# Kernel tuning notes

Measured on AMD Instinct MI355X. Metric: run time of the kernel, lower is better.

The kernel has to match this reference:

```python
import jax, jax.numpy as jnp
import numpy as np
import math

ROPE_BASE = 10000.0
ALIBI_SLOPE = 2.0 ** (-8.0)  # _get_alibi_slopes(1) == [2**(-8*1/1)]


def _rope_cos_sin(T, d):
    inv_freq = 1.0 / (ROPE_BASE ** (jnp.arange(0, d, 2, dtype=jnp.float32) / d))
    t = jnp.arange(T, dtype=jnp.float32)
    freqs = jnp.einsum('i,j->ij', t, inv_freq)          # [T, d/2]
    emb = jnp.concatenate([freqs, freqs], axis=-1)      # [T, d]
    return jnp.cos(emb), jnp.sin(emb)


def _rotate_half(x):
    x1, x2 = jnp.split(x, 2, axis=-1)
    return jnp.concatenate([-x2, x1], axis=-1)


def setup_inputs() -> dict:
    key = jax.random.key(0)
    kq, kk, kv = jax.random.split(key, 3)
    B, T, H = 8, 2048, 256
    return {
        'q': jax.random.normal(kq, (B, T, H), dtype=jnp.float32),
        'k': jax.random.normal(kk, (B, T, H), dtype=jnp.float32),
        'v': jax.random.normal(kv, (B, T, H), dtype=jnp.float32),
    }


def reference(q, k, v):
    B, T, H = q.shape  # num_heads == 1, so head_dim == H
    cos, sin = _rope_cos_sin(T, H)                      # [T, H]
    qe = q * cos + _rotate_half(q) * sin                # [B, T, H]
    ke = k * cos + _rotate_half(k) * sin                # [B, T, H]

    scale = 1.0 / math.sqrt(H)
    scores = jnp.einsum('btd,bsd->bts', qe, ke) * scale  # [B, T, T]

    pos = jnp.arange(T)
    rel = (pos[None, :] - pos[:, None]).astype(jnp.float32)  # [T, T]
    alibi = (ALIBI_SLOPE * rel)[None, None, :, :]            # [1, 1, T, T]

    # torch broadcast: [B,T,T] + [1,1,T,T] -> [1,B,T,T]
    scores = scores + alibi
    attn = jax.nn.softmax(scores, axis=-1)              # [1, B, T, T]
    out = jnp.matmul(attn, v)                           # [1, B, T, H]
    return out
```

## Files before the change

kernel.cpp:

```cpp
#include <hip/hip_runtime.h>

#define B_ 8
#define T_ 2048
#define H_ 256
#define PSTR 40
#define SCALE2 0.0901684403f
#define SLOPE2 0.00563552752f

typedef __attribute__((ext_vector_type(8))) short bf16x8;
typedef __attribute__((ext_vector_type(4))) float f32x4;

#define MFMA16(a, b, c) __builtin_amdgcn_mfma_f32_16x16x32_bf16((a), (b), (c), 0, 0, 0)

__device__ __forceinline__ ushort f2bf(float f) {
  unsigned u = __float_as_uint(f);
  u += 0x7FFFu + ((u >> 16) & 1u);
  return (ushort)(u >> 16);
}

__device__ __forceinline__ void gl_lds16(const ushort* g, ushort* l) {
  __builtin_amdgcn_global_load_lds(
      (const __attribute__((address_space(1))) unsigned int*)g,
      (__attribute__((address_space(3))) unsigned int*)l, 16, 0, 0);
}

__global__ void prep_kernel(const float* __restrict__ k, const float* __restrict__ v,
                            ushort* __restrict__ kt, ushort* __restrict__ vt) {
  __shared__ ushort tile[64][72];
  const int bid = blockIdx.x;
  const int tid = threadIdx.x;
  if (bid < 4096) {
    int idx = bid * 256 + tid;
    int jp = idx & 63, bt = idx >> 6;
    int t = bt & (T_ - 1);
    int b = bt >> 11;
    int j = jp * 2;
    float rv0 = (float)t * exp2f((float)j * -0.103810252959f) * 0.15915494309f;
    float rv1 = (float)t * exp2f((float)(j + 1) * -0.103810252959f) * 0.15915494309f;
    float fr0 = rv0 - floorf(rv0), fr1 = rv1 - floorf(rv1);
    float sn0 = __builtin_amdgcn_sinf(fr0), cs0 = __builtin_amdgcn_cosf(fr0);
    float sn1 = __builtin_amdgcn_sinf(fr1), cs1 = __builtin_amdgcn_cosf(fr1);
    size_t base = (size_t)bt * H_ + j;
    float2 a = *(const float2*)(k + base);
    float2 c = *(const float2*)(k + base + 128);
    ushort2 lo, hi;
    lo.x = f2bf(a.x * cs0 - c.x * sn0); lo.y = f2bf(a.y * cs1 - c.y * sn1);
    hi.x = f2bf(c.x * cs0 + a.x * sn0); hi.y = f2bf(c.y * cs1 + a.y * sn1);
    size_t kdst = (((size_t)(b * 64 + (t >> 5)) * 32 + (j >> 3)) * 32 + (t & 31)) * 8 + (j & 7);
    *(ushort2*)(kt + kdst) = lo;
    *(ushort2*)(kt + kdst + 4096) = hi;
  } else {
    int bid2 = bid - 4096;
    int b = bid2 >> 7, rem = bid2 & 127;
    int h0 = (rem >> 5) * 64, t0 = (rem & 31) * 64;
    int c4 = tid & 15, r0 = tid >> 4;
#pragma unroll
    for (int p = 0; p < 4; ++p) {
      int row = r0 + p * 16;
      const float4 f = *(const float4*)(v + ((size_t)(b * T_ + t0 + row)) * H_ + h0 + c4 * 4);
      ushort4 u;
      u.x = f2bf(f.x); u.y = f2bf(f.y); u.z = f2bf(f.z); u.w = f2bf(f.w);
      *(ushort4*)&tile[row][(c4 * 4) ^ (8 * ((row >> 3) & 7))] = u;
    }
    __syncthreads();
#pragma unroll
    for (int p = 0; p < 2; ++p) {
      int c = tid + p * 256;
      int h = c >> 3, tc = (c & 7) * 8;
      int xo = 8 * (c & 7);
      ushort4 u0, u1;
      u0.x = tile[tc + 0][h ^ xo]; u0.y = tile[tc + 1][h ^ xo];
      u0.z = tile[tc + 2][h ^ xo]; u0.w = tile[tc + 3][h ^ xo];
      u1.x = tile[tc + 4][h ^ xo]; u1.y = tile[tc + 5][h ^ xo];
      u1.z = tile[tc + 6][h ^ xo]; u1.w = tile[tc + 7][h ^ xo];
      int tg = t0 + tc;
      size_t dst = (((size_t)(b * 64 + (tg >> 5)) * 4 + ((tg >> 3) & 3)) * 256 + (h0 + h)) * 8;
      *(ushort4*)(vt + dst) = u0;
      *(ushort4*)(vt + dst + 4) = u1;
    }
  }
}

__global__ __launch_bounds__(128, 1)
void attn_kernel(const float* __restrict__ q, const ushort* __restrict__ kt,
                 const ushort* __restrict__ vt, float* __restrict__ out,
                 float* __restrict__ o1, float* __restrict__ lpart) {
  __shared__ ushort Ksh[2][8192];
  __shared__ ushort Vsh[8192];
  __shared__ ushort Psh[2][32 * PSTR];

  const int tid = threadIdx.x;
  const int w = tid >> 6, lane = tid & 63, quad = lane >> 4, l16 = lane & 15;
  const int b = blockIdx.x;
  const int q0 = blockIdx.y * 64;
  const int sp = blockIdx.z;
  const int kvb = sp * (T_ / 2);

  bf16x8 aq[2][8];
  {
    const float* qb = q + ((size_t)(b * T_) + q0 + w * 32) * H_;
#pragma unroll
    for (int mt = 0; mt < 2; ++mt) {
      int t = q0 + w * 32 + mt * 16 + l16;
      float qv[8][8];
#pragma unroll
      for (int ks = 0; ks < 8; ++ks) {
        float4 x0 = *(const float4*)(qb + (size_t)(mt * 16 + l16) * H_ + ks * 32 + quad * 8);
        float4 x1 = *(const float4*)(qb + (size_t)(mt * 16 + l16) * H_ + ks * 32 + quad * 8 + 4);
        qv[ks][0] = x0.x; qv[ks][1] = x0.y; qv[ks][2] = x0.z; qv[ks][3] = x0.w;
        qv[ks][4] = x1.x; qv[ks][5] = x1.y; qv[ks][6] = x1.z; qv[ks][7] = x1.w;
      }
#pragma unroll
      for (int ks = 0; ks < 4; ++ks)
#pragma unroll
        for (int e = 0; e < 8; ++e) {
          int d = ks * 32 + quad * 8 + e;
          float rv = (float)t * exp2f((float)d * -0.103810252959f) * 0.15915494309f;
          float fr = rv - floorf(rv);
          float sn = __builtin_amdgcn_sinf(fr), cs = __builtin_amdgcn_cosf(fr);
          aq[mt][ks][e]     = (short)f2bf(qv[ks][e] * cs - qv[ks + 4][e] * sn);
          aq[mt][ks + 4][e] = (short)f2bf(qv[ks + 4][e] * cs + qv[ks][e] * sn);
        }
    }
  }

  const f32x4 fzero = {0.f, 0.f, 0.f, 0.f};
  f32x4 O[2][16], lac[2];
#pragma unroll
  for (int mt = 0; mt < 2; ++mt) {
    lac[mt] = fzero;
#pragma unroll
    for (int ht = 0; ht < 16; ++ht) O[mt][ht] = fzero;
  }
  bf16x8 vones;
#pragma unroll
  for (int i = 0; i < 8; ++i) vones[i] = (short)0x3F80;

  const ushort* ktb = kt + (size_t)(b * 64 + sp * 32) * 8192;
  const ushort* vtb = vt + (size_t)(b * 64 + sp * 32) * 8192;
  const int stoff = w * 4096 + lane * 8;

#pragma unroll
  for (int i = 0; i < 8; ++i)
    gl_lds16(ktb + stoff + i * 512, &Ksh[0][stoff + i * 512]);
  __builtin_amdgcn_sched_barrier(0);
  __builtin_amdgcn_s_waitcnt(0x0070);
  __builtin_amdgcn_s_barrier();
  __builtin_amdgcn_sched_barrier(0);

  const float arb = SLOPE2 * (float)(q0 + w * 32 + quad * 4);

  for (int it = 0; it < 32; ++it) {
    const int p = it & 1;
    {
      const ushort* vg = vtb + (size_t)it * 8192;
#pragma unroll
      for (int i = 0; i < 8; ++i)
        gl_lds16(vg + stoff + i * 512, &Vsh[stoff + i * 512]);
      const int itn = (it < 31) ? it + 1 : 31;
      const ushort* kg = ktb + (size_t)itn * 8192;
#pragma unroll
      for (int i = 0; i < 8; ++i)
        gl_lds16(kg + stoff + i * 512, &Ksh[1 - p][stoff + i * 512]);
    }
    __builtin_amdgcn_sched_barrier(0);

    f32x4 s[2][2] = {{fzero, fzero}, {fzero, fzero}};
#pragma unroll
    for (int ks = 0; ks < 8; ++ks)
#pragma unroll
      for (int nt = 0; nt < 2; ++nt) {
        bf16x8 kf = *(const bf16x8*)&Ksh[p][((ks * 4 + quad) * 32 + nt * 16 + l16) * 8];
        s[0][nt] = MFMA16(aq[0][ks], kf, s[0][nt]);
        s[1][nt] = MFMA16(aq[1][ks], kf, s[1][nt]);
      }

    __builtin_amdgcn_sched_barrier(0);
    __builtin_amdgcn_s_waitcnt(0x0F78);
    __builtin_amdgcn_s_barrier();
    __builtin_amdgcn_sched_barrier(0);

#pragma unroll
    for (int nt = 0; nt < 2; ++nt) {
      float ac = SLOPE2 * (float)(kvb + it * 32 + nt * 16 + l16);
#pragma unroll
      for (int mt = 0; mt < 2; ++mt)
#pragma unroll
        for (int r = 0; r < 4; ++r) {
          float a0 = ac - arb - SLOPE2 * (float)(mt * 16 + r);
          float pv = __builtin_amdgcn_exp2f(fmaf(s[mt][nt][r], SCALE2, a0));
          Psh[w][(mt * 16 + quad * 4 + r) * PSTR + nt * 16 + l16] = f2bf(pv);
        }
    }

    bf16x8 pf0 = *(const bf16x8*)&Psh[w][l16 * PSTR + quad * 8];
    bf16x8 pf1 = *(const bf16x8*)&Psh[w][(16 + l16) * PSTR + quad * 8];
    lac[0] = MFMA16(pf0, vones, lac[0]);
    lac[1] = MFMA16(pf1, vones, lac[1]);
#pragma unroll
    for (int ht = 0; ht < 16; ++ht) {
      bf16x8 vf = *(const bf16x8*)&Vsh[(quad * 256 + ht * 16 + l16) * 8];
      O[0][ht] = MFMA16(pf0, vf, O[0][ht]);
      O[1][ht] = MFMA16(pf1, vf, O[1][ht]);
    }

    __builtin_amdgcn_sched_barrier(0);
    __builtin_amdgcn_s_waitcnt(0x0070);
    __builtin_amdgcn_s_barrier();
    __builtin_amdgcn_sched_barrier(0);
  }

  float* od = (sp == 0) ? out : o1;
  float* ob = od + ((size_t)(b * T_) + q0 + w * 32) * H_;
#pragma unroll
  for (int mt = 0; mt < 2; ++mt)
#pragma unroll
    for (int r = 0; r < 4; ++r) {
      int row = mt * 16 + quad * 4 + r;
#pragma unroll
      for (int ht = 0; ht < 16; ++ht)
        ob[(size_t)row * H_ + ht * 16 + l16] = O[mt][ht][r];
    }
  if (l16 == 0) {
#pragma unroll
    for (int mt = 0; mt < 2; ++mt)
#pragma unroll
      for (int r = 0; r < 4; ++r)
        lpart[(size_t)(sp * B_ + b) * T_ + q0 + w * 32 + mt * 16 + quad * 4 + r] =
            lac[mt][r];
  }
}

__global__ void combine_kernel(float* __restrict__ out, const float* __restrict__ o1,
                               const float* __restrict__ lpart) {
  int idx = blockIdx.x * 256 + threadIdx.x;
  int row = idx >> 6;
  float inv = 1.0f / (lpart[row] + lpart[B_ * T_ + row]);
  float4 a = ((const float4*)out)[idx];
  float4 c = ((const float4*)o1)[idx];
  a.x = (a.x + c.x) * inv; a.y = (a.y + c.y) * inv;
  a.z = (a.z + c.z) * inv; a.w = (a.w + c.w) * inv;
  ((float4*)out)[idx] = a;
}

extern "C" void kernel_launch(void* const* d_in, const int* in_sizes, int n_in,
                              void* d_out, int out_size, void* d_ws, size_t ws_size,
                              hipStream_t stream) {
  const float* q = (const float*)d_in[0];
  const float* k = (const float*)d_in[1];
  const float* v = (const float*)d_in[2];
  float* out = (float*)d_out;

  const size_t elems = (size_t)B_ * T_ * H_;
  ushort* kt = (ushort*)d_ws;
  ushort* vt = kt + elems;
  float* o1 = (float*)(vt + elems);
  float* lpart = o1 + elems;

  prep_kernel<<<dim3(5120), 256, 0, stream>>>(k, v, kt, vt);
  attn_kernel<<<dim3(B_, T_ / 64, 2), 128, 0, stream>>>(q, kt, vt, out, o1, lpart);
  combine_kernel<<<dim3((B_ * T_ * H_ / 4) / 256), 256, 0, stream>>>(out, o1, lpart);
}
```

Before: 164.8 us.

## Use 8-wave blocks of 128 queries with double-buffered K/V prefetch

The attention kernel moves from 2 waves covering 64 query rows, 32 rows each, to 8 waves covering 128 query rows, 16 rows each. Each K/V tile loaded into LDS is now shared by four times as many query rows. V is now double-buffered like K, and tiles are prefetched two iterations ahead, leaving one barrier per iteration instead of two. The price is more LDS, fewer MFMAs per LDS fragment read since each wave handles one 16-row tile, and half as many blocks in the grid (256).

```diff
diff --git a/kernel.cpp b/kernel.cpp
--- a/kernel.cpp
+++ b/kernel.cpp
@@ -81,153 +81,134 @@
   }
 }
 
-__global__ __launch_bounds__(128, 1)
+__global__ __launch_bounds__(512, 2)
 void attn_kernel(const float* __restrict__ q, const ushort* __restrict__ kt,
                  const ushort* __restrict__ vt, float* __restrict__ out,
                  float* __restrict__ o1, float* __restrict__ lpart) {
   __shared__ ushort Ksh[2][8192];
-  __shared__ ushort Vsh[8192];
-  __shared__ ushort Psh[2][32 * PSTR];
+  __shared__ ushort Vsh[2][8192];
+  __shared__ ushort Psh[8][16 * PSTR];
 
   const int tid = threadIdx.x;
   const int w = tid >> 6, lane = tid & 63, quad = lane >> 4, l16 = lane & 15;
   const int b = blockIdx.x;
-  const int q0 = blockIdx.y * 64;
+  const int q0 = blockIdx.y * 128;
   const int sp = blockIdx.z;
   const int kvb = sp * (T_ / 2);
 
-  bf16x8 aq[2][8];
+  bf16x8 aq[8];
   {
-    const float* qb = q + ((size_t)(b * T_) + q0 + w * 32) * H_;
-#pragma unroll
-    for (int mt = 0; mt < 2; ++mt) {
-      int t = q0 + w * 32 + mt * 16 + l16;
-      float qv[8][8];
-#pragma unroll
-      for (int ks = 0; ks < 8; ++ks) {
-        float4 x0 = *(const float4*)(qb + (size_t)(mt * 16 + l16) * H_ + ks * 32 + quad * 8);
-        float4 x1 = *(const float4*)(qb + (size_t)(mt * 16 + l16) * H_ + ks * 32 + quad * 8 + 4);
-        qv[ks][0] = x0.x; qv[ks][1] = x0.y; qv[ks][2] = x0.z; qv[ks][3] = x0.w;
-        qv[ks][4] = x1.x; qv[ks][5] = x1.y; qv[ks][6] = x1.z; qv[ks][7] = x1.w;
+    const float* qb = q + ((size_t)(b * T_) + q0 + w * 16) * H_;
+    const int t = q0 + w * 16 + l16;
+    float qv[8][8];
+#pragma unroll
+    for (int ks = 0; ks < 8; ++ks) {
+      float4 x0 = *(const float4*)(qb + (size_t)l16 * H_ + ks * 32 + quad * 8);
+      float4 x1 = *(const float4*)(qb + (size_t)l16 * H_ + ks * 32 + quad * 8 + 4);
+      qv[ks][0] = x0.x; qv[ks][1] = x0.y; qv[ks][2] = x0.z; qv[ks][3] = x0.w;
+      qv[ks][4] = x1.x; qv[ks][5] = x1.y; qv[ks][6] = x1.z; qv[ks][7] = x1.w;
+    }
+#pragma unroll
+    for (int ks = 0; ks < 4; ++ks)
+#pragma unroll
+      for (int e = 0; e < 8; ++e) {
+        int d = ks * 32 + quad * 8 + e;
+        float rv = (float)t * exp2f((float)d * -0.103810252959f) * 0.15915494309f;
+        float fr = rv - floorf(rv);
+        float sn = __builtin_amdgcn_sinf(fr), cs = __builtin_amdgcn_cosf(fr);
+        aq[ks][e]     = (short)f2bf(qv[ks][e] * cs - qv[ks + 4][e] * sn);
+        aq[ks + 4][e] = (short)f2bf(qv[ks + 4][e] * cs + qv[ks][e] * sn);
       }
-#pragma unroll
-      for (int ks = 0; ks < 4; ++ks)
-#pragma unroll
-        for (int e = 0; e < 8; ++e) {
-          int d = ks * 32 + quad * 8 + e;
-          float rv = (float)t * exp2f((float)d * -0.103810252959f) * 0.15915494309f;
-          float fr = rv - floorf(rv);
-          float sn = __builtin_amdgcn_sinf(fr), cs = __builtin_amdgcn_cosf(fr);
-          aq[mt][ks][e]     = (short)f2bf(qv[ks][e] * cs - qv[ks + 4][e] * sn);
-          aq[mt][ks + 4][e] = (short)f2bf(qv[ks + 4][e] * cs + qv[ks][e] * sn);
-        }
-    }
   }
 
   const f32x4 fzero = {0.f, 0.f, 0.f, 0.f};
-  f32x4 O[2][16], lac[2];
-#pragma unroll
-  for (int mt = 0; mt < 2; ++mt) {
-    lac[mt] = fzero;
-#pragma unroll
-    for (int ht = 0; ht < 16; ++ht) O[mt][ht] = fzero;
-  }
+  f32x4 O[16], lac = fzero;
+#pragma unroll
+  for (int ht = 0; ht < 16; ++ht) O[ht] = fzero;
   bf16x8 vones;
 #pragma unroll
   for (int i = 0; i < 8; ++i) vones[i] = (short)0x3F80;
 
   const ushort* ktb = kt + (size_t)(b * 64 + sp * 32) * 8192;
   const ushort* vtb = vt + (size_t)(b * 64 + sp * 32) * 8192;
-  const int stoff = w * 4096 + lane * 8;
-
-#pragma unroll
-  for (int i = 0; i < 8; ++i)
-    gl_lds16(ktb + stoff + i * 512, &Ksh[0][stoff + i * 512]);
-  __builtin_amdgcn_sched_barrier(0);
-  __builtin_amdgcn_s_waitcnt(0x0070);
-  __builtin_amdgcn_s_barrier();
-  __builtin_amdgcn_sched_barrier(0);
-
-  const float arb = SLOPE2 * (float)(q0 + w * 32 + quad * 4);
+  const int stoff = tid * 8;
+
+#pragma unroll
+  for (int tt = 0; tt < 2; ++tt) {
+    const ushort* kg = ktb + (size_t)tt * 8192;
+    const ushort* vg = vtb + (size_t)tt * 8192;
+    gl_lds16(kg + stoff, &Ksh[tt][stoff]);
+    gl_lds16(kg + stoff + 4096, &Ksh[tt][stoff + 4096]);
+    gl_lds16(vg + stoff, &Vsh[tt][stoff]);
+    gl_lds16(vg + stoff + 4096, &Vsh[tt][stoff + 4096]);
+  }
+
+  const float arb = SLOPE2 * (float)(q0 + w * 16 + quad * 4);
 
   for (int it = 0; it < 32; ++it) {
     const int p = it & 1;
-    {
-      const ushort* vg = vtb + (size_t)it * 8192;
-#pragma unroll
-      for (int i = 0; i < 8; ++i)
-        gl_lds16(vg + stoff + i * 512, &Vsh[stoff + i * 512]);
-      const int itn = (it < 31) ? it + 1 : 31;
-      const ushort* kg = ktb + (size_t)itn * 8192;
-#pragma unroll
-      for (int i = 0; i < 8; ++i)
-        gl_lds16(kg + stoff + i * 512, &Ksh[1 - p][stoff + i * 512]);
-    }
-    __builtin_amdgcn_sched_barrier(0);
-
-    f32x4 s[2][2] = {{fzero, fzero}, {fzero, fzero}};
+    __builtin_amdgcn_sched_barrier(0);
+    if (it == 31) __builtin_amdgcn_s_waitcnt(0x0070);
+    else          __builtin_amdgcn_s_waitcnt(0x0F74);
+    __builtin_amdgcn_s_barrier();
+    __builtin_amdgcn_sched_barrier(0);
+
+    f32x4 s[2] = {fzero, fzero};
 #pragma unroll
     for (int ks = 0; ks < 8; ++ks)
 #pragma unroll
       for (int nt = 0; nt < 2; ++nt) {
         bf16x8 kf = *(const bf16x8*)&Ksh[p][((ks * 4 + quad) * 32 + nt * 16 + l16) * 8];
-        s[0][nt] = MFMA16(aq[0][ks], kf, s[0][nt]);
-        s[1][nt] = MFMA16(aq[1][ks], kf, s[1][nt]);
+        s[nt] = MFMA16(aq[ks], kf, s[nt]);
       }
-
-    __builtin_amdgcn_sched_barrier(0);
-    __builtin_amdgcn_s_waitcnt(0x0F78);
-    __builtin_amdgcn_s_barrier();
-    __builtin_amdgcn_sched_barrier(0);
 
 #pragma unroll
     for (int nt = 0; nt < 2; ++nt) {
       float ac = SLOPE2 * (float)(kvb + it * 32 + nt * 16 + l16);
 #pragma unroll
-      for (int mt = 0; mt < 2; ++mt)
-#pragma unroll
-        for (int r = 0; r < 4; ++r) {
-          float a0 = ac - arb - SLOPE2 * (float)(mt * 16 + r);
-          float pv = __builtin_amdgcn_exp2f(fmaf(s[mt][nt][r], SCALE2, a0));
-          Psh[w][(mt * 16 + quad * 4 + r) * PSTR + nt * 16 + l16] = f2bf(pv);
-        }
-    }
-
-    bf16x8 pf0 = *(const bf16x8*)&Psh[w][l16 * PSTR + quad * 8];
-    bf16x8 pf1 = *(const bf16x8*)&Psh[w][(16 + l16) * PSTR + quad * 8];
-    lac[0] = MFMA16(pf0, vones, lac[0]);
-    lac[1] = MFMA16(pf1, vones, lac[1]);
+      for (int r = 0; r < 4; ++r) {
+        float a0 = ac - arb - SLOPE2 * (float)r;
+        float pv = __builtin_amdgcn_exp2f(fmaf(s[nt][r], SCALE2, a0));
+        Psh[w][(quad * 4 + r) * PSTR + nt * 16 + l16] = f2bf(pv);
+      }
+    }
+
+    bf16x8 pf = *(const bf16x8*)&Psh[w][l16 * PSTR + quad * 8];
+    lac = MFMA16(pf, vones, lac);
 #pragma unroll
     for (int ht = 0; ht < 16; ++ht) {
-      bf16x8 vf = *(const bf16x8*)&Vsh[(quad * 256 + ht * 16 + l16) * 8];
-      O[0][ht] = MFMA16(pf0, vf, O[0][ht]);
-      O[1][ht] = MFMA16(pf1, vf, O[1][ht]);
-    }
-
-    __builtin_amdgcn_sched_barrier(0);
-    __builtin_amdgcn_s_waitcnt(0x0070);
+      bf16x8 vf = *(const bf16x8*)&Vsh[p][(quad * 256 + ht * 16 + l16) * 8];
+      O[ht] = MFMA16(pf, vf, O[ht]);
+    }
+
+    __builtin_amdgcn_sched_barrier(0);
+    __builtin_amdgcn_s_waitcnt(0xC07F);
     __builtin_amdgcn_s_barrier();
     __builtin_amdgcn_sched_barrier(0);
+
+    if (it < 30) {
+      const ushort* kg = ktb + (size_t)(it + 2) * 8192;
+      const ushort* vg = vtb + (size_t)(it + 2) * 8192;
+      gl_lds16(kg + stoff, &Ksh[p][stoff]);
+      gl_lds16(kg + stoff + 4096, &Ksh[p][stoff + 4096]);
+      gl_lds16(vg + stoff, &Vsh[p][stoff]);
+      gl_lds16(vg + stoff + 4096, &Vsh[p][stoff + 4096]);
+    }
   }
 
   float* od = (sp == 0) ? out : o1;
-  float* ob = od + ((size_t)(b * T_) + q0 + w * 32) * H_;
-#pragma unroll
-  for (int mt = 0; mt < 2; ++mt)
-#pragma unroll
-    for (int r = 0; r < 4; ++r) {
-      int row = mt * 16 + quad * 4 + r;
-#pragma unroll
-      for (int ht = 0; ht < 16; ++ht)
-        ob[(size_t)row * H_ + ht * 16 + l16] = O[mt][ht][r];
-    }
+  float* ob = od + ((size_t)(b * T_) + q0 + w * 16) * H_;
+#pragma unroll
+  for (int r = 0; r < 4; ++r) {
+    int row = quad * 4 + r;
+#pragma unroll
+    for (int ht = 0; ht < 16; ++ht)
+      ob[(size_t)row * H_ + ht * 16 + l16] = O[ht][r];
+  }
   if (l16 == 0) {
 #pragma unroll
-    for (int mt = 0; mt < 2; ++mt)
-#pragma unroll
-      for (int r = 0; r < 4; ++r)
-        lpart[(size_t)(sp * B_ + b) * T_ + q0 + w * 32 + mt * 16 + quad * 4 + r] =
-            lac[mt][r];
+    for (int r = 0; r < 4; ++r)
+      lpart[(size_t)(sp * B_ + b) * T_ + q0 + w * 16 + quad * 4 + r] = lac[r];
   }
 }
 
@@ -258,6 +239,6 @@
   float* lpart = o1 + elems;
 
   prep_kernel<<<dim3(5120), 256, 0, stream>>>(k, v, kt, vt);
-  attn_kernel<<<dim3(B_, T_ / 64, 2), 128, 0, stream>>>(q, kt, vt, out, o1, lpart);
+  attn_kernel<<<dim3(B_, T_ / 128, 2), 512, 0, stream>>>(q, kt, vt, out, o1, lpart);
   combine_kernel<<<dim3((B_ * T_ * H_ / 4) / 256), 256, 0, stream>>>(out, o1, lpart);
 }
```

After: 151.5 us. 8.1% less time.

## Double-buffer K/V with 4-wave blocks, split-KV into 4, vectorize K prep

Applied to the files above, without the earlier changes.

Attention blocks grow to four waves covering 128 query rows. K and V are both double-buffered and prefetched two tiles ahead, with a single barrier per iteration and s_setprio raised around the MFMA bursts. The KV dimension is split into up to four parts when workspace allows, and the combine kernel sums a variable number of partials. K rotary prep now handles eight elements per thread with 16-byte stores. The aim is better latency hiding and occupancy, at the cost of more LDS per block and extra partial-output traffic in combine.

```diff
diff --git a/kernel.cpp b/kernel.cpp
--- a/kernel.cpp
+++ b/kernel.cpp
@@ -6,6 +6,7 @@
 #define PSTR 40
 #define SCALE2 0.0901684403f
 #define SLOPE2 0.00563552752f
+#define ELEMS ((size_t)B_ * T_ * H_)
 
 typedef __attribute__((ext_vector_type(8))) short bf16x8;
 typedef __attribute__((ext_vector_type(4))) float f32x4;
@@ -29,28 +30,34 @@
   __shared__ ushort tile[64][72];
   const int bid = blockIdx.x;
   const int tid = threadIdx.x;
-  if (bid < 4096) {
+  if (bid < 1024) {
     int idx = bid * 256 + tid;
-    int jp = idx & 63, bt = idx >> 6;
+    int d8 = idx & 15;
+    int bt = idx >> 4;
     int t = bt & (T_ - 1);
     int b = bt >> 11;
-    int j = jp * 2;
-    float rv0 = (float)t * exp2f((float)j * -0.103810252959f) * 0.15915494309f;
-    float rv1 = (float)t * exp2f((float)(j + 1) * -0.103810252959f) * 0.15915494309f;
-    float fr0 = rv0 - floorf(rv0), fr1 = rv1 - floorf(rv1);
-    float sn0 = __builtin_amdgcn_sinf(fr0), cs0 = __builtin_amdgcn_cosf(fr0);
-    float sn1 = __builtin_amdgcn_sinf(fr1), cs1 = __builtin_amdgcn_cosf(fr1);
-    size_t base = (size_t)bt * H_ + j;
-    float2 a = *(const float2*)(k + base);
-    float2 c = *(const float2*)(k + base + 128);
-    ushort2 lo, hi;
-    lo.x = f2bf(a.x * cs0 - c.x * sn0); lo.y = f2bf(a.y * cs1 - c.y * sn1);
-    hi.x = f2bf(c.x * cs0 + a.x * sn0); hi.y = f2bf(c.y * cs1 + a.y * sn1);
-    size_t kdst = (((size_t)(b * 64 + (t >> 5)) * 32 + (j >> 3)) * 32 + (t & 31)) * 8 + (j & 7);
-    *(ushort2*)(kt + kdst) = lo;
-    *(ushort2*)(kt + kdst + 4096) = hi;
+    size_t base = (size_t)bt * H_ + d8 * 8;
+    float4 a0 = *(const float4*)(k + base);
+    float4 a1 = *(const float4*)(k + base + 4);
+    float4 c0 = *(const float4*)(k + base + 128);
+    float4 c1 = *(const float4*)(k + base + 132);
+    float av[8] = {a0.x, a0.y, a0.z, a0.w, a1.x, a1.y, a1.z, a1.w};
+    float cv[8] = {c0.x, c0.y, c0.z, c0.w, c1.x, c1.y, c1.z, c1.w};
+    bf16x8 lo, hi;
+#pragma unroll
+    for (int e = 0; e < 8; ++e) {
+      int j = d8 * 8 + e;
+      float rv = (float)t * exp2f((float)j * -0.103810252959f) * 0.15915494309f;
+      float fr = rv - floorf(rv);
+      float sn = __builtin_amdgcn_sinf(fr), cs = __builtin_amdgcn_cosf(fr);
+      lo[e] = (short)f2bf(av[e] * cs - cv[e] * sn);
+      hi[e] = (short)f2bf(cv[e] * cs + av[e] * sn);
+    }
+    size_t kdst = (((size_t)(b * 64 + (t >> 5)) * 32 + d8) * 32 + (t & 31)) * 8;
+    *(bf16x8*)(kt + kdst) = lo;
+    *(bf16x8*)(kt + kdst + 4096) = hi;
   } else {
-    int bid2 = bid - 4096;
+    int bid2 = bid - 1024;
     int b = bid2 >> 7, rem = bid2 & 127;
     int h0 = (rem >> 5) * 64, t0 = (rem & 31) * 64;
     int c4 = tid & 15, r0 = tid >> 4;
@@ -81,20 +88,22 @@
   }
 }
 
-__global__ __launch_bounds__(128, 1)
+__global__ __launch_bounds__(256, 2)
 void attn_kernel(const float* __restrict__ q, const ushort* __restrict__ kt,
                  const ushort* __restrict__ vt, float* __restrict__ out,
-                 float* __restrict__ o1, float* __restrict__ lpart) {
+                 float* __restrict__ opart, float* __restrict__ lpart) {
   __shared__ ushort Ksh[2][8192];
-  __shared__ ushort Vsh[8192];
-  __shared__ ushort Psh[2][32 * PSTR];
+  __shared__ ushort Vsh[2][8192];
+  __shared__ ushort Psh[4][32 * PSTR];
 
   const int tid = threadIdx.x;
   const int w = tid >> 6, lane = tid & 63, quad = lane >> 4, l16 = lane & 15;
   const int b = blockIdx.x;
-  const int q0 = blockIdx.y * 64;
+  const int q0 = blockIdx.y * 128;
   const int sp = blockIdx.z;
-  const int kvb = sp * (T_ / 2);
+  const int S = gridDim.z;
+  const int niter = (T_ / 32) / S;
+  const int kvb = sp * (T_ / S);
 
   bf16x8 aq[2][8];
   {
@@ -136,36 +145,33 @@
 #pragma unroll
   for (int i = 0; i < 8; ++i) vones[i] = (short)0x3F80;
 
-  const ushort* ktb = kt + (size_t)(b * 64 + sp * 32) * 8192;
-  const ushort* vtb = vt + (size_t)(b * 64 + sp * 32) * 8192;
-  const int stoff = w * 4096 + lane * 8;
-
-#pragma unroll
-  for (int i = 0; i < 8; ++i)
-    gl_lds16(ktb + stoff + i * 512, &Ksh[0][stoff + i * 512]);
-  __builtin_amdgcn_sched_barrier(0);
-  __builtin_amdgcn_s_waitcnt(0x0070);
-  __builtin_amdgcn_s_barrier();
-  __builtin_amdgcn_sched_barrier(0);
+  const ushort* ktb = kt + (size_t)(b * 64 + sp * niter) * 8192;
+  const ushort* vtb = vt + (size_t)(b * 64 + sp * niter) * 8192;
+  const int stoff = tid * 8;
+
+#pragma unroll
+  for (int tt = 0; tt < 2; ++tt) {
+    const ushort* kg = ktb + (size_t)tt * 8192;
+    const ushort* vg = vtb + (size_t)tt * 8192;
+#pragma unroll
+    for (int i = 0; i < 4; ++i) {
+      gl_lds16(kg + stoff + i * 2048, &Ksh[tt][stoff + i * 2048]);
+      gl_lds16(vg + stoff + i * 2048, &Vsh[tt][stoff + i * 2048]);
+    }
+  }
 
   const float arb = SLOPE2 * (float)(q0 + w * 32 + quad * 4);
 
-  for (int it = 0; it < 32; ++it) {
+  for (int it = 0; it < niter; ++it) {
     const int p = it & 1;
-    {
-      const ushort* vg = vtb + (size_t)it * 8192;
-#pragma unroll
-      for (int i = 0; i < 8; ++i)
-        gl_lds16(vg + stoff + i * 512, &Vsh[stoff + i * 512]);
-      const int itn = (it < 31) ? it + 1 : 31;
-      const ushort* kg = ktb + (size_t)itn * 8192;
-#pragma unroll
-      for (int i = 0; i < 8; ++i)
-        gl_lds16(kg + stoff + i * 512, &Ksh[1 - p][stoff + i * 512]);
-    }
+    __builtin_amdgcn_sched_barrier(0);
+    if (it == niter - 1) __builtin_amdgcn_s_waitcnt(0x0070);
+    else                 __builtin_amdgcn_s_waitcnt(0x0F78);
+    __builtin_amdgcn_s_barrier();
     __builtin_amdgcn_sched_barrier(0);
 
     f32x4 s[2][2] = {{fzero, fzero}, {fzero, fzero}};
+    __builtin_amdgcn_s_setprio(1);
 #pragma unroll
     for (int ks = 0; ks < 8; ++ks)
 #pragma unroll
@@ -174,11 +180,7 @@
         s[0][nt] = MFMA16(aq[0][ks], kf, s[0][nt]);
         s[1][nt] = MFMA16(aq[1][ks], kf, s[1][nt]);
       }
-
-    __builtin_amdgcn_sched_barrier(0);
-    __builtin_amdgcn_s_waitcnt(0x0F78);
-    __builtin_amdgcn_s_barrier();
-    __builtin_amdgcn_sched_barrier(0);
+    __builtin_amdgcn_s_setprio(0);
 
 #pragma unroll
     for (int nt = 0; nt < 2; ++nt) {
@@ -195,22 +197,34 @@
 
     bf16x8 pf0 = *(const bf16x8*)&Psh[w][l16 * PSTR + quad * 8];
     bf16x8 pf1 = *(const bf16x8*)&Psh[w][(16 + l16) * PSTR + quad * 8];
+    __builtin_amdgcn_s_setprio(1);
     lac[0] = MFMA16(pf0, vones, lac[0]);
     lac[1] = MFMA16(pf1, vones, lac[1]);
 #pragma unroll
     for (int ht = 0; ht < 16; ++ht) {
-      bf16x8 vf = *(const bf16x8*)&Vsh[(quad * 256 + ht * 16 + l16) * 8];
+      bf16x8 vf = *(const bf16x8*)&Vsh[p][(quad * 256 + ht * 16 + l16) * 8];
       O[0][ht] = MFMA16(pf0, vf, O[0][ht]);
       O[1][ht] = MFMA16(pf1, vf, O[1][ht]);
     }
-
-    __builtin_amdgcn_sched_barrier(0);
-    __builtin_amdgcn_s_waitcnt(0x0070);
+    __builtin_amdgcn_s_setprio(0);
+
+    __builtin_amdgcn_sched_barrier(0);
+    __builtin_amdgcn_s_waitcnt(0xC07F);
     __builtin_amdgcn_s_barrier();
     __builtin_amdgcn_sched_barrier(0);
-  }
-
-  float* od = (sp == 0) ? out : o1;
+
+    if (it < niter - 2) {
+      const ushort* kg = ktb + (size_t)(it + 2) * 8192;
+      const ushort* vg = vtb + (size_t)(it + 2) * 8192;
+#pragma unroll
+      for (int i = 0; i < 4; ++i) {
+        gl_lds16(kg + stoff + i * 2048, &Ksh[p][stoff + i * 2048]);
+        gl_lds16(vg + stoff + i * 2048, &Vsh[p][stoff + i * 2048]);
+      }
+    }
+  }
+
+  float* od = (sp == 0) ? out : (opart + (size_t)(sp - 1) * ELEMS);
   float* ob = od + ((size_t)(b * T_) + q0 + w * 32) * H_;
 #pragma unroll
   for (int mt = 0; mt < 2; ++mt)
@@ -231,15 +245,19 @@
   }
 }
 
-__global__ void combine_kernel(float* __restrict__ out, const float* __restrict__ o1,
-                               const float* __restrict__ lpart) {
+__global__ void combine_kernel(float* __restrict__ out, const float* __restrict__ opart,
+                               const float* __restrict__ lpart, int S) {
   int idx = blockIdx.x * 256 + threadIdx.x;
   int row = idx >> 6;
-  float inv = 1.0f / (lpart[row] + lpart[B_ * T_ + row]);
+  float l = lpart[row];
+  for (int s = 1; s < S; ++s) l += lpart[(size_t)s * B_ * T_ + row];
+  float inv = 1.0f / l;
   float4 a = ((const float4*)out)[idx];
-  float4 c = ((const float4*)o1)[idx];
-  a.x = (a.x + c.x) * inv; a.y = (a.y + c.y) * inv;
-  a.z = (a.z + c.z) * inv; a.w = (a.w + c.w) * inv;
+  for (int s = 1; s < S; ++s) {
+    float4 c = ((const float4*)opart)[(size_t)(s - 1) * (ELEMS / 4) + idx];
+    a.x += c.x; a.y += c.y; a.z += c.z; a.w += c.w;
+  }
+  a.x *= inv; a.y *= inv; a.z *= inv; a.w *= inv;
   ((float4*)out)[idx] = a;
 }
 
@@ -251,13 +269,14 @@
   const float* v = (const float*)d_in[2];
   float* out = (float*)d_out;
 
-  const size_t elems = (size_t)B_ * T_ * H_;
   ushort* kt = (ushort*)d_ws;
-  ushort* vt = kt + elems;
-  float* o1 = (float*)(vt + elems);
-  float* lpart = o1 + elems;
-
-  prep_kernel<<<dim3(5120), 256, 0, stream>>>(k, v, kt, vt);
-  attn_kernel<<<dim3(B_, T_ / 64, 2), 128, 0, stream>>>(q, kt, vt, out, o1, lpart);
-  combine_kernel<<<dim3((B_ * T_ * H_ / 4) / 256), 256, 0, stream>>>(out, o1, lpart);
-}
+  ushort* vt = kt + ELEMS;
+  float* opart = (float*)(vt + ELEMS);
+  const size_t need4 = ELEMS * 4 + 3 * ELEMS * 4 + (size_t)4 * B_ * T_ * 4;
+  const int S = (ws_size >= need4) ? 4 : 2;
+  float* lpart = opart + (size_t)(S - 1) * ELEMS;
+
+  prep_kernel<<<dim3(2048), 256, 0, stream>>>(k, v, kt, vt);
+  attn_kernel<<<dim3(B_, T_ / 128, S), 256, 0, stream>>>(q, kt, vt, out, opart, lpart);
+  combine_kernel<<<dim3((B_ * T_ * H_ / 4) / 256), 256, 0, stream>>>(out, opart, lpart, S);
+}
```

New measurement: 152.3 us. 1.08x faster.
